# Performance work log

Measured on AMD Instinct MI355X. Metric: run time of the kernel, lower is better.

Reference implementation:

```python
import jax, jax.numpy as jnp
import numpy as np

LN_EPS = 1e-3  # keras LayerNormalization default epsilon


def setup_inputs() -> dict:
    key = jax.random.key(0)
    ks = jax.random.split(key, 6)
    B, S, D, H, K = 4, 4096, 1024, 16, 64
    scale = 1.0 / np.sqrt(D)
    return {
        "x": jax.random.normal(ks[0], (B, S, D), jnp.float32),
        "Wq": jax.random.normal(ks[1], (D, H, K), jnp.float32) * scale,
        "bq": jnp.zeros((H, K), jnp.float32),
        "Wk": jax.random.normal(ks[2], (D, H, K), jnp.float32) * scale,
        "bk": jnp.zeros((H, K), jnp.float32),
        "Wv": jax.random.normal(ks[3], (D, H, K), jnp.float32) * scale,
        "bv": jnp.zeros((H, K), jnp.float32),
        "Wo": jax.random.normal(ks[4], (H, K, D), jnp.float32) * scale,
        "bo": jnp.zeros((D,), jnp.float32),
        "gamma": jnp.ones((D,), jnp.float32),
        "beta": jnp.zeros((D,), jnp.float32),
        "num_window": 8,
    }


def reference(x, Wq, bq, Wk, bk, Wv, bv, Wo, bo, gamma, beta, num_window):
    B, S, D = x.shape
    H, K = Wq.shape[1], Wq.shape[2]
    Sw = S // num_window
    # Block-diagonal (windowed) attention: reshape seq into windows instead of a Python loop.
    xw = x.reshape(B, num_window, Sw, D)  # [B, W, Sw, D]
    q = jnp.einsum('bwsd,dhk->bwshk', xw, Wq) + bq
    k = jnp.einsum('bwsd,dhk->bwshk', xw, Wk) + bk
    v = jnp.einsum('bwsd,dhk->bwshk', xw, Wv) + bv
    scores = jnp.einsum('bwqhk,bwshk->bwhqs', q, k) / jnp.sqrt(jnp.asarray(K, x.dtype))
    attn = jax.nn.softmax(scores, axis=-1)  # [B, W, H, Sw, Sw]
    ctx = jnp.einsum('bwhqs,bwshk->bwqhk', attn, v)
    attn_out = (jnp.einsum('bwqhk,hkd->bwqd', ctx, Wo) + bo).reshape(B, S, D)
    # residual + layernorm (keras eps=1e-3)
    y = x + attn_out
    mu = jnp.mean(y, axis=-1, keepdims=True)
    var = jnp.mean(jnp.square(y - mu), axis=-1, keepdims=True)
    return (y - mu) * jax.lax.rsqrt(var + LN_EPS) * gamma + beta
```

## Files before the change

kernel.cpp:

```cpp
#include <hip/hip_runtime.h>

typedef __bf16 bf16_t;
typedef __bf16 bf16x4 __attribute__((ext_vector_type(4)));
typedef __bf16 bf16x8 __attribute__((ext_vector_type(8)));
typedef float f32x4 __attribute__((ext_vector_type(4)));

#define MFMA16(a, b, c) __builtin_amdgcn_mfma_f32_16x16x32_bf16((a), (b), (c), 0, 0, 0)

#define FENCE asm volatile("" ::: "memory")
#define BAR()                        \
  do {                               \
    FENCE;                           \
    __builtin_amdgcn_s_barrier();    \
    FENCE;                           \
  } while (0)
#define WAITLGKM(n) asm volatile("s_waitcnt lgkmcnt(" #n ")" ::: "memory")

__device__ __forceinline__ void gl_lds16(const bf16_t* g, bf16_t* l) {
  __builtin_amdgcn_global_load_lds(
      (const __attribute__((address_space(1))) void*)g,
      (__attribute__((address_space(3))) void*)l, 16, 0, 0);
}

__global__ __launch_bounds__(256) void cast_x_kernel(const float* __restrict__ x,
                                                     bf16_t* __restrict__ xb) {
  size_t i = (size_t)blockIdx.x * 256 + threadIdx.x;
  float4 v = ((const float4*)x)[i];
  bf16x4 o = {(bf16_t)v.x, (bf16_t)v.y, (bf16_t)v.z, (bf16_t)v.w};
  ((bf16x4*)xb)[i] = o;
}

__global__ __launch_bounds__(256) void transpose_w_kernel(
    const float* __restrict__ Wq, const float* __restrict__ Wk,
    const float* __restrict__ Wv, const float* __restrict__ Wo,
    bf16_t* __restrict__ Wt, bf16_t* __restrict__ WoT) {
  __shared__ bf16_t T[64 * 68];
  const int z = blockIdx.z;
  const float* src = (z == 0) ? Wq : (z == 1) ? Wk : (z == 2) ? Wv : Wo;
  bf16_t* dst = (z < 3) ? (Wt + (size_t)z * 1024 * 1024) : WoT;
  const int tr = blockIdx.y * 64;
  const int tc = blockIdx.x * 64;
  const int tid = threadIdx.x;
#pragma unroll
  for (int it = 0; it < 4; ++it) {
    int t = tid + it * 256;
    int row = t >> 4, c4 = t & 15;
    float4 v = *(const float4*)&src[(size_t)(tr + row) * 1024 + tc + c4 * 4];
    bf16x4 o = {(bf16_t)v.x, (bf16_t)v.y, (bf16_t)v.z, (bf16_t)v.w};
    *(bf16x4*)&T[row * 68 + c4 * 4] = o;
  }
  __syncthreads();
#pragma unroll
  for (int it = 0; it < 2; ++it) {
    int t = tid + it * 256;
    int n = t >> 3, d8 = t & 7;
    bf16x8 o;
#pragma unroll
    for (int j = 0; j < 8; ++j) o[j] = T[(d8 * 8 + j) * 68 + n];
    *(bf16x8*)&dst[(size_t)(tc + n) * 1024 + tr + d8 * 8] = o;
  }
}


__device__ __forceinline__ void stage_half(const bf16_t* __restrict__ g,
                                           bf16_t* l, const int tid) {
#pragma unroll
  for (int j = 0; j < 2; ++j) {
    int idx = j * 512 + tid;
    int row = idx >> 3;
    int c = (idx & 7) ^ (row & 7);
    gl_lds16(g + (size_t)row * 1024 + c * 8, l + idx * 8);
  }
}

__device__ __forceinline__ void tile_step(const int t, bf16_t* const buf,
                                          bf16_t* const nbuf,
                                          const bf16_t* __restrict__ Ab,
                                          const bf16_t* __restrict__ Bb,
                                          f32x4 (&acc)[8][4], const int tid) {
  const int l15 = tid & 15, quad = (tid >> 4) & 3;
  const int wv = tid >> 6, wm = wv >> 2, wn = wv & 3;
  const int sx = l15 & 7;
  const int brow0 = (wn & 1) * 64;
  const bf16_t* const Ar = buf + wm * 8192;
  const bf16_t* const Br = buf + (2 + (wn >> 1)) * 8192;

  bf16x8 af[4][2], bfr[4][2];

#pragma unroll
  for (int nf = 0; nf < 2; ++nf)
#pragma unroll
    for (int ks = 0; ks < 2; ++ks)
      bfr[nf][ks] = *(const bf16x8*)&Br[(brow0 + nf * 16 + l15) * 64 +
                                        (((ks * 4 + quad) ^ sx) << 3)];
  FENCE;
#pragma unroll
  for (int mf = 0; mf < 2; ++mf)
#pragma unroll
    for (int ks = 0; ks < 2; ++ks)
      af[mf][ks] = *(const bf16x8*)&Ar[(mf * 16 + l15) * 64 +
                                       (((ks * 4 + quad) ^ sx) << 3)];
  FENCE;
#pragma unroll
  for (int mf = 2; mf < 4; ++mf)
#pragma unroll
    for (int ks = 0; ks < 2; ++ks)
      af[mf][ks] = *(const bf16x8*)&Ar[(mf * 16 + l15) * 64 +
                                       (((ks * 4 + quad) ^ sx) << 3)];
  FENCE;
#pragma unroll
  for (int nf = 2; nf < 4; ++nf)
#pragma unroll
    for (int ks = 0; ks < 2; ++ks)
      bfr[nf][ks] = *(const bf16x8*)&Br[(brow0 + nf * 16 + l15) * 64 +
                                        (((ks * 4 + quad) ^ sx) << 3)];
  FENCE;
  if (t + 1 < 16) {
    stage_half(Bb + 128 * 1024 + (t + 1) * 64, nbuf + 3 * 8192, tid);
    stage_half(Ab + 128 * 1024 + (t + 1) * 64, nbuf + 1 * 8192, tid);
  }

  WAITLGKM(8);
  __builtin_amdgcn_s_setprio(1);
#pragma unroll
  for (int ks = 0; ks < 2; ++ks)
#pragma unroll
    for (int mf = 0; mf < 2; ++mf)
#pragma unroll
      for (int nf = 0; nf < 2; ++nf)
        acc[mf][nf] = MFMA16(af[mf][ks], bfr[nf][ks], acc[mf][nf]);
  __builtin_amdgcn_s_setprio(0);

  WAITLGKM(4);
  __builtin_amdgcn_s_setprio(1);
#pragma unroll
  for (int ks = 0; ks < 2; ++ks)
#pragma unroll
    for (int mf = 2; mf < 4; ++mf)
#pragma unroll
      for (int nf = 0; nf < 2; ++nf)
        acc[mf][nf] = MFMA16(af[mf][ks], bfr[nf][ks], acc[mf][nf]);
  __builtin_amdgcn_s_setprio(0);

  WAITLGKM(0);
  __builtin_amdgcn_s_setprio(1);
#pragma unroll
  for (int ks = 0; ks < 2; ++ks)
#pragma unroll
    for (int mf = 0; mf < 4; ++mf)
#pragma unroll
      for (int nf = 2; nf < 4; ++nf)
        acc[mf][nf] = MFMA16(af[mf][ks], bfr[nf][ks], acc[mf][nf]);
  __builtin_amdgcn_s_setprio(0);
  BAR();

  if (t + 2 < 16) stage_half(Bb + (t + 2) * 64, buf + 2 * 8192, tid);
#pragma unroll
  for (int mf = 0; mf < 2; ++mf)
#pragma unroll
    for (int ks = 0; ks < 2; ++ks)
      af[mf][ks] = *(const bf16x8*)&Ar[((mf + 4) * 16 + l15) * 64 +
                                       (((ks * 4 + quad) ^ sx) << 3)];
  FENCE;
#pragma unroll
  for (int mf = 2; mf < 4; ++mf)
#pragma unroll
    for (int ks = 0; ks < 2; ++ks)
      af[mf][ks] = *(const bf16x8*)&Ar[((mf + 4) * 16 + l15) * 64 +
                                       (((ks * 4 + quad) ^ sx) << 3)];
  FENCE;
  WAITLGKM(4);
  __builtin_amdgcn_s_setprio(1);
#pragma unroll
  for (int ks = 0; ks < 2; ++ks)
#pragma unroll
    for (int mf = 0; mf < 2; ++mf)
#pragma unroll
      for (int nf = 2; nf < 4; ++nf)
        acc[mf + 4][nf] = MFMA16(af[mf][ks], bfr[nf][ks], acc[mf + 4][nf]);
  __builtin_amdgcn_s_setprio(0);
  WAITLGKM(0);
  __builtin_amdgcn_s_setprio(1);
#pragma unroll
  for (int ks = 0; ks < 2; ++ks)
#pragma unroll
    for (int mf = 2; mf < 4; ++mf)
#pragma unroll
      for (int nf = 2; nf < 4; ++nf)
        acc[mf + 4][nf] = MFMA16(af[mf][ks], bfr[nf][ks], acc[mf + 4][nf]);
  __builtin_amdgcn_s_setprio(0);
  BAR();

  if (t + 2 < 16) stage_half(Ab + (t + 2) * 64, buf + 0 * 8192, tid);
  __builtin_amdgcn_s_setprio(1);
#pragma unroll
  for (int ks = 0; ks < 2; ++ks)
#pragma unroll
    for (int mf = 0; mf < 4; ++mf)
#pragma unroll
      for (int nf = 0; nf < 2; ++nf)
        acc[mf + 4][nf] = MFMA16(af[mf][ks], bfr[nf][ks], acc[mf + 4][nf]);
  __builtin_amdgcn_s_setprio(0);
  if (t < 14)
    asm volatile("s_waitcnt vmcnt(4)" ::: "memory");
  else
    asm volatile("s_waitcnt vmcnt(0)" ::: "memory");
  BAR();
}

__device__ __forceinline__ void gemm256_main(const bf16_t* __restrict__ Ab,
                                             const bf16_t* __restrict__ Bb,
                                             bf16_t* lds, f32x4 (&acc)[8][4],
                                             const int tid) {
  stage_half(Bb, lds + 2 * 8192, tid);
  stage_half(Ab, lds + 0 * 8192, tid);
  stage_half(Bb + 128 * 1024, lds + 3 * 8192, tid);
  stage_half(Ab + 128 * 1024, lds + 1 * 8192, tid);
  stage_half(Bb + 64, lds + 6 * 8192, tid);
  stage_half(Ab + 64, lds + 4 * 8192, tid);
  asm volatile("s_waitcnt vmcnt(4)" ::: "memory");
  BAR();

  for (int t = 0; t < 16; t += 2) {
    tile_step(t, lds, lds + 32768, Ab, Bb, acc, tid);
    tile_step(t + 1, lds + 32768, lds, Ab, Bb, acc, tid);
  }
}

__global__ __launch_bounds__(512, 2) void gemm_qkv_kernel(
    const bf16_t* __restrict__ A, const bf16_t* __restrict__ Bt,
    const float* __restrict__ bq, const float* __restrict__ bk,
    const float* __restrict__ bv, bf16_t* __restrict__ C) {
  __shared__ bf16_t lds[2 * 4 * 8192];
  const int tid = threadIdx.x;
  const int lin = blockIdx.x;
  const int swz = (lin & 7) * 96 + (lin >> 3);
  const int bm = swz / 12, bn = swz - bm * 12;

  f32x4 acc[8][4];
#pragma unroll
  for (int i = 0; i < 8; ++i)
#pragma unroll
    for (int j = 0; j < 4; ++j)
#pragma unroll
      for (int e = 0; e < 4; ++e) acc[i][j][e] = 0.f;

  gemm256_main(A + (size_t)(bm * 256) * 1024, Bt + (size_t)(bn * 256) * 1024,
               lds, acc, tid);

  const int l15 = tid & 15, quad = (tid >> 4) & 3;
  const int wv = tid >> 6, wm = wv >> 2, wn = wv & 3;
  const int col0 = bn * 256 + wn * 64;
  const int rbase = bm * 256 + wm * 128;
  float* R = (float*)(lds + wv * 8192);

  float wbias[4], wscale[4];
#pragma unroll
  for (int nf = 0; nf < 4; ++nf) {
    int col = col0 + nf * 16 + l15;
    if (col < 1024) {
      wbias[nf] = bq[col];
      wscale[nf] = 0.125f;
    } else if (col < 2048) {
      wbias[nf] = bk[col - 1024];
      wscale[nf] = 1.f;
    } else {
      wbias[nf] = bv[col - 2048];
      wscale[nf] = 1.f;
    }
  }
#pragma unroll
  for (int p = 0; p < 4; ++p) {
#pragma unroll
    for (int mfi = 0; mfi < 2; ++mfi) {
#pragma unroll
      for (int nf = 0; nf < 4; ++nf)
#pragma unroll
        for (int r = 0; r < 4; ++r)
          R[(mfi * 16 + quad * 4 + r) * 68 + nf * 16 + l15] =
              (acc[p * 2 + mfi][nf][r] + wbias[nf]) * wscale[nf];
    }
    WAITLGKM(0);
#pragma unroll
    for (int i = 0; i < 8; ++i) {
      const int lr = i * 4 + quad;
      f32x4 vv = *(const f32x4*)&R[lr * 68 + l15 * 4];
      bf16x4 o = {(bf16_t)vv[0], (bf16_t)vv[1], (bf16_t)vv[2], (bf16_t)vv[3]};
      int row = rbase + p * 32 + lr;
      *(bf16x4*)&C[(size_t)row * 3072 + col0 + l15 * 4] = o;
    }
    WAITLGKM(0);
  }
}

__global__ __launch_bounds__(256) void attn_kernel(
    const bf16_t* __restrict__ QKV, bf16_t* __restrict__ Ctx) {
  __shared__ bf16_t Ks[2][64 * 64];
  __shared__ bf16_t Vs[2][64 * 64];
  __shared__ bf16_t Pb[4][16 * 64];

  const int tid = threadIdx.x;
  const int wv = tid >> 6, quad = (tid >> 4) & 3, l15 = tid & 15;
  const int hid = blockIdx.x, qb = blockIdx.y;
  const int b = hid >> 7, w = (hid >> 4) & 7, h = hid & 15;
  const int rowW = b * 4096 + w * 512;
  const int qbase = qb * 128 + wv * 32;

  bf16x8 qf[2][2];
#pragma unroll
  for (int qt = 0; qt < 2; ++qt) {
    int rowQ = rowW + qbase + qt * 16 + l15;
#pragma unroll
    for (int kh = 0; kh < 2; ++kh)
      qf[qt][kh] = *(const bf16x8*)&QKV[(size_t)rowQ * 3072 + h * 64 + kh * 32 + quad * 8];
  }

  const bf16_t* Kb = QKV + (size_t)rowW * 3072 + 1024 + h * 64;
  const bf16_t* Vg = QKV + (size_t)rowW * 3072 + 2048 + h * 64;

  float lp[2] = {0.f, 0.f};
  f32x4 Oa[2][4];
  f32x4 zero = {0.f, 0.f, 0.f, 0.f};
#pragma unroll
  for (int qt = 0; qt < 2; ++qt)
#pragma unroll
    for (int dt = 0; dt < 4; ++dt) Oa[qt][dt] = zero;

  const int vrow = tid >> 2;
  const int vseg = tid & 3;
  const int sg = vrow >> 3, sr = vrow & 7;

  bf16x8 vr0, vr1;
  {
    const bf16_t* src = Vg + (size_t)vrow * 3072 + vseg * 16;
    vr0 = *(const bf16x8*)&src[0];
    vr1 = *(const bf16x8*)&src[8];
  }
  FENCE;
#pragma unroll
  for (int i = 0; i < 2; ++i) {
    int t = tid + i * 256;
    int row = t >> 3;
    int g = (t & 7) ^ (row & 7);
    gl_lds16(Kb + (size_t)row * 3072 + g * 8, &Ks[0][t * 8]);
  }
  FENCE;

#pragma unroll 2
  for (int kt = 0; kt < 8; ++kt) {
    const int cb = kt & 1;
    bf16x8 vn0 = vr0, vn1 = vr1;
    if (kt < 7) {
      const bf16_t* src = Vg + (size_t)((kt + 1) * 64 + vrow) * 3072 + vseg * 16;
      vn0 = *(const bf16x8*)&src[0];
      vn1 = *(const bf16x8*)&src[8];
      FENCE;
#pragma unroll
      for (int i = 0; i < 2; ++i) {
        int t = tid + i * 256;
        int row = t >> 3;
        int g = (t & 7) ^ (row & 7);
        gl_lds16(Kb + (size_t)((kt + 1) * 64 + row) * 3072 + g * 8, &Ks[cb ^ 1][t * 8]);
      }
      asm volatile("s_waitcnt vmcnt(4)" ::: "memory");
    } else {
      asm volatile("s_waitcnt vmcnt(0)" ::: "memory");
    }
#pragma unroll
    for (int j = 0; j < 8; ++j) {
      int d0 = vseg * 16 + j;
      Vs[cb][d0 * 64 + ((sg ^ (d0 & 7)) << 3) + sr] = vr0[j];
      int d1 = vseg * 16 + 8 + j;
      Vs[cb][d1 * 64 + ((sg ^ (d1 & 7)) << 3) + sr] = vr1[j];
    }
    WAITLGKM(0);
    BAR();

    bf16x8 kf[4][2], vf[2][4];
#pragma unroll
    for (int jt = 0; jt < 4; ++jt) {
      int key = jt * 16 + l15;
#pragma unroll
      for (int kh = 0; kh < 2; ++kh)
        kf[jt][kh] = *(const bf16x8*)&Ks[cb][key * 64 + (((kh * 4 + quad) ^ (key & 7)) << 3)];
    }
#pragma unroll
    for (int kh = 0; kh < 2; ++kh)
#pragma unroll
      for (int dt = 0; dt < 4; ++dt) {
        int d = dt * 16 + l15;
        vf[kh][dt] = *(const bf16x8*)&Vs[cb][d * 64 + (((kh * 4 + quad) ^ (d & 7)) << 3)];
      }

#pragma unroll
    for (int qt = 0; qt < 2; ++qt) {
      f32x4 st[4];
#pragma unroll
      for (int jt = 0; jt < 4; ++jt) {
        f32x4 a = zero;
#pragma unroll
        for (int kh = 0; kh < 2; ++kh) a = MFMA16(kf[jt][kh], qf[qt][kh], a);
        st[jt] = a;
      }
      float ls = 0.f;
#pragma unroll
      for (int jt = 0; jt < 4; ++jt)
#pragma unroll
        for (int r = 0; r < 4; ++r) {
          float p = __expf(st[jt][r]);
          st[jt][r] = p;
          ls += p;
        }
      lp[qt] += ls;
#pragma unroll
      for (int jt = 0; jt < 4; ++jt) {
        bf16x4 pk = {(bf16_t)st[jt][0], (bf16_t)st[jt][1],
                     (bf16_t)st[jt][2], (bf16_t)st[jt][3]};
        int gs = (jt * 2 + (quad >> 1)) ^ (l15 & 7);
        *(bf16x4*)&Pb[wv][l15 * 64 + gs * 8 + (quad & 1) * 4] = pk;
      }
#pragma unroll
      for (int kh = 0; kh < 2; ++kh) {
        bf16x8 pf = *(const bf16x8*)&Pb[wv][l15 * 64 + (((kh * 4 + quad) ^ (l15 & 7)) << 3)];
#pragma unroll
        for (int dt = 0; dt < 4; ++dt) Oa[qt][dt] = MFMA16(pf, vf[kh][dt], Oa[qt][dt]);
      }
    }
    WAITLGKM(0);
    BAR();
    vr0 = vn0;
    vr1 = vn1;
  }

#pragma unroll
  for (int qt = 0; qt < 2; ++qt) {
    float t = lp[qt];
    t += __shfl_xor(t, 16, 64);
    t += __shfl_xor(t, 32, 64);
    float inv_l = 1.0f / t;
    float inv[4];
#pragma unroll
    for (int r = 0; r < 4; ++r) inv[r] = __shfl(inv_l, quad * 4 + r, 64);
#pragma unroll
    for (int dt = 0; dt < 4; ++dt)
#pragma unroll
      for (int r = 0; r < 4; ++r) {
        int orow = rowW + qbase + qt * 16 + quad * 4 + r;
        Ctx[(size_t)orow * 1024 + h * 64 + dt * 16 + l15] = (bf16_t)(Oa[qt][dt][r] * inv[r]);
      }
  }
}

__global__ __launch_bounds__(512, 2) void gemm_proj_kernel(
    const bf16_t* __restrict__ A, const bf16_t* __restrict__ Bt,
    const float* __restrict__ bo, const float* __restrict__ x,
    bf16_t* __restrict__ Yb) {
  __shared__ bf16_t lds[2 * 4 * 8192];
  const int tid = threadIdx.x;
  const int lin = blockIdx.x;
  const int swz = (lin & 7) * 32 + (lin >> 3);
  const int bm = swz >> 2, bn = swz & 3;

  f32x4 acc[8][4];
#pragma unroll
  for (int i = 0; i < 8; ++i)
#pragma unroll
    for (int j = 0; j < 4; ++j)
#pragma unroll
      for (int e = 0; e < 4; ++e) acc[i][j][e] = 0.f;

  gemm256_main(A + (size_t)(bm * 256) * 1024, Bt + (size_t)(bn * 256) * 1024,
               lds, acc, tid);

  const int l15 = tid & 15, quad = (tid >> 4) & 3;
  const int wv = tid >> 6, wm = wv >> 2, wn = wv & 3;
  const int col0 = bn * 256 + wn * 64;
  const int rbase = bm * 256 + wm * 128;
  float* R = (float*)(lds + wv * 8192);
  const int colg = col0 + l15 * 4;
  const float4 bo4 = *(const float4*)&bo[colg];

#pragma unroll
  for (int p = 0; p < 4; ++p) {
#pragma unroll
    for (int mfi = 0; mfi < 2; ++mfi) {
#pragma unroll
      for (int nf = 0; nf < 4; ++nf)
#pragma unroll
        for (int r = 0; r < 4; ++r)
          R[(mfi * 16 + quad * 4 + r) * 68 + nf * 16 + l15] = acc[p * 2 + mfi][nf][r];
    }
    WAITLGKM(0);
#pragma unroll
    for (int i = 0; i < 8; ++i) {
      const int lr = i * 4 + quad;
      int row = rbase + p * 32 + lr;
      f32x4 vv = *(const f32x4*)&R[lr * 68 + l15 * 4];
      float4 xv = *(const float4*)&x[(size_t)row * 1024 + colg];
      bf16x4 o = {(bf16_t)(vv[0] + bo4.x + xv.x), (bf16_t)(vv[1] + bo4.y + xv.y),
                  (bf16_t)(vv[2] + bo4.z + xv.z), (bf16_t)(vv[3] + bo4.w + xv.w)};
      *(bf16x4*)&Yb[(size_t)row * 1024 + colg] = o;
    }
    WAITLGKM(0);
  }
}

__global__ __launch_bounds__(256) void ln_kernel(const bf16_t* __restrict__ Yb,
                                                 float* __restrict__ Y,
                                                 const float* __restrict__ gamma,
                                                 const float* __restrict__ beta) {
  const int row = blockIdx.x, tid = threadIdx.x;
  bf16x4 yb = ((const bf16x4*)(Yb + (size_t)row * 1024))[tid];
  float y0 = (float)yb[0], y1 = (float)yb[1], y2 = (float)yb[2], y3 = (float)yb[3];
  float s = y0 + y1 + y2 + y3;
  float s2 = y0 * y0 + y1 * y1 + y2 * y2 + y3 * y3;
#pragma unroll
  for (int off = 1; off < 64; off <<= 1) {
    s += __shfl_xor(s, off, 64);
    s2 += __shfl_xor(s2, off, 64);
  }
  __shared__ float red[8];
  int wv = tid >> 6;
  if ((tid & 63) == 0) {
    red[wv] = s;
    red[4 + wv] = s2;
  }
  __syncthreads();
  s = red[0] + red[1] + red[2] + red[3];
  s2 = red[4] + red[5] + red[6] + red[7];
  float mean = s * (1.0f / 1024.0f);
  float var = s2 * (1.0f / 1024.0f) - mean * mean;
  float rs = rsqrtf(var + 1e-3f);
  float4 g = ((const float4*)gamma)[tid];
  float4 bb = ((const float4*)beta)[tid];
  float4 o;
  o.x = (y0 - mean) * rs * g.x + bb.x;
  o.y = (y1 - mean) * rs * g.y + bb.y;
  o.z = (y2 - mean) * rs * g.z + bb.z;
  o.w = (y3 - mean) * rs * g.w + bb.w;
  ((float4*)(Y + (size_t)row * 1024))[tid] = o;
}

extern "C" void kernel_launch(void* const* d_in, const int* in_sizes, int n_in,
                              void* d_out, int out_size, void* d_ws, size_t ws_size,
                              hipStream_t stream) {
  const float* x = (const float*)d_in[0];
  const float* Wq = (const float*)d_in[1];
  const float* bq = (const float*)d_in[2];
  const float* Wk = (const float*)d_in[3];
  const float* bk = (const float*)d_in[4];
  const float* Wv = (const float*)d_in[5];
  const float* bv = (const float*)d_in[6];
  const float* Wo = (const float*)d_in[7];
  const float* bo = (const float*)d_in[8];
  const float* gamma = (const float*)d_in[9];
  const float* beta = (const float*)d_in[10];
  float* Y = (float*)d_out;

  char* ws = (char*)d_ws;
  bf16_t* xb = (bf16_t*)(ws);
  bf16_t* Wt = (bf16_t*)(ws + 33554432);
  bf16_t* WoT = (bf16_t*)(ws + 39845888);
  bf16_t* QKVb = (bf16_t*)(ws + 41943040);
  bf16_t* Ctx = (bf16_t*)(ws + 142606336);
  bf16_t* Yb = (bf16_t*)(ws + 176160768);

  cast_x_kernel<<<16384, 256, 0, stream>>>(x, xb);
  transpose_w_kernel<<<dim3(16, 16, 4), 256, 0, stream>>>(Wq, Wk, Wv, Wo, Wt, WoT);
  gemm_qkv_kernel<<<768, 512, 0, stream>>>(xb, Wt, bq, bk, bv, QKVb);
  attn_kernel<<<dim3(512, 4), 256, 0, stream>>>(QKVb, Ctx);
  gemm_proj_kernel<<<256, 512, 0, stream>>>(Ctx, WoT, bo, x, Yb);
  ln_kernel<<<16384, 256, 0, stream>>>(Yb, Y, gamma, beta);
}
```

Measured before the change: 365.9 us.

## Restructure GEMM main-loop interleaving with extra barriers and swizzle attention grid

```diff
diff --git a/kernel.cpp b/kernel.cpp
--- a/kernel.cpp
+++ b/kernel.cpp
@@ -95,19 +95,27 @@
                                         (((ks * 4 + quad) ^ sx) << 3)];
   FENCE;
 #pragma unroll
-  for (int mf = 0; mf < 2; ++mf)
+  for (int mf = 0; mf < 4; ++mf)
 #pragma unroll
     for (int ks = 0; ks < 2; ++ks)
       af[mf][ks] = *(const bf16x8*)&Ar[(mf * 16 + l15) * 64 +
                                        (((ks * 4 + quad) ^ sx) << 3)];
   FENCE;
-#pragma unroll
-  for (int mf = 2; mf < 4; ++mf)
-#pragma unroll
-    for (int ks = 0; ks < 2; ++ks)
-      af[mf][ks] = *(const bf16x8*)&Ar[(mf * 16 + l15) * 64 +
-                                       (((ks * 4 + quad) ^ sx) << 3)];
-  FENCE;
+  if (t + 1 < 16) stage_half(Bb + 128 * 1024 + (t + 1) * 64, nbuf + 3 * 8192, tid);
+  WAITLGKM(8);
+  BAR();
+  WAITLGKM(0);
+  __builtin_amdgcn_s_setprio(1);
+#pragma unroll
+  for (int ks = 0; ks < 2; ++ks)
+#pragma unroll
+    for (int mf = 0; mf < 4; ++mf)
+#pragma unroll
+      for (int nf = 0; nf < 2; ++nf)
+        acc[mf][nf] = MFMA16(af[mf][ks], bfr[nf][ks], acc[mf][nf]);
+  __builtin_amdgcn_s_setprio(0);
+  BAR();
+
 #pragma unroll
   for (int nf = 2; nf < 4; ++nf)
 #pragma unroll
@@ -115,33 +123,8 @@
       bfr[nf][ks] = *(const bf16x8*)&Br[(brow0 + nf * 16 + l15) * 64 +
                                         (((ks * 4 + quad) ^ sx) << 3)];
   FENCE;
-  if (t + 1 < 16) {
-    stage_half(Bb + 128 * 1024 + (t + 1) * 64, nbuf + 3 * 8192, tid);
-    stage_half(Ab + 128 * 1024 + (t + 1) * 64, nbuf + 1 * 8192, tid);
-  }
-
-  WAITLGKM(8);
-  __builtin_amdgcn_s_setprio(1);
-#pragma unroll
-  for (int ks = 0; ks < 2; ++ks)
-#pragma unroll
-    for (int mf = 0; mf < 2; ++mf)
-#pragma unroll
-      for (int nf = 0; nf < 2; ++nf)
-        acc[mf][nf] = MFMA16(af[mf][ks], bfr[nf][ks], acc[mf][nf]);
-  __builtin_amdgcn_s_setprio(0);
-
-  WAITLGKM(4);
-  __builtin_amdgcn_s_setprio(1);
-#pragma unroll
-  for (int ks = 0; ks < 2; ++ks)
-#pragma unroll
-    for (int mf = 2; mf < 4; ++mf)
-#pragma unroll
-      for (int nf = 0; nf < 2; ++nf)
-        acc[mf][nf] = MFMA16(af[mf][ks], bfr[nf][ks], acc[mf][nf]);
-  __builtin_amdgcn_s_setprio(0);
-
+  if (t + 1 < 16) stage_half(Ab + 128 * 1024 + (t + 1) * 64, nbuf + 1 * 8192, tid);
+  BAR();
   WAITLGKM(0);
   __builtin_amdgcn_s_setprio(1);
 #pragma unroll
@@ -154,44 +137,29 @@
   __builtin_amdgcn_s_setprio(0);
   BAR();
 
-  if (t + 2 < 16) stage_half(Bb + (t + 2) * 64, buf + 2 * 8192, tid);
-#pragma unroll
-  for (int mf = 0; mf < 2; ++mf)
+#pragma unroll
+  for (int mf = 0; mf < 4; ++mf)
 #pragma unroll
     for (int ks = 0; ks < 2; ++ks)
       af[mf][ks] = *(const bf16x8*)&Ar[((mf + 4) * 16 + l15) * 64 +
                                        (((ks * 4 + quad) ^ sx) << 3)];
   FENCE;
-#pragma unroll
-  for (int mf = 2; mf < 4; ++mf)
-#pragma unroll
-    for (int ks = 0; ks < 2; ++ks)
-      af[mf][ks] = *(const bf16x8*)&Ar[((mf + 4) * 16 + l15) * 64 +
-                                       (((ks * 4 + quad) ^ sx) << 3)];
-  FENCE;
-  WAITLGKM(4);
+  if (t + 2 < 16) stage_half(Bb + (t + 2) * 64, buf + 2 * 8192, tid);
+  BAR();
+  WAITLGKM(0);
   __builtin_amdgcn_s_setprio(1);
 #pragma unroll
   for (int ks = 0; ks < 2; ++ks)
 #pragma unroll
-    for (int mf = 0; mf < 2; ++mf)
+    for (int mf = 0; mf < 4; ++mf)
 #pragma unroll
       for (int nf = 2; nf < 4; ++nf)
         acc[mf + 4][nf] = MFMA16(af[mf][ks], bfr[nf][ks], acc[mf + 4][nf]);
   __builtin_amdgcn_s_setprio(0);
-  WAITLGKM(0);
-  __builtin_amdgcn_s_setprio(1);
-#pragma unroll
-  for (int ks = 0; ks < 2; ++ks)
-#pragma unroll
-    for (int mf = 2; mf < 4; ++mf)
-#pragma unroll
-      for (int nf = 2; nf < 4; ++nf)
-        acc[mf + 4][nf] = MFMA16(af[mf][ks], bfr[nf][ks], acc[mf + 4][nf]);
-  __builtin_amdgcn_s_setprio(0);
   BAR();
 
   if (t + 2 < 16) stage_half(Ab + (t + 2) * 64, buf + 0 * 8192, tid);
+  BAR();
   __builtin_amdgcn_s_setprio(1);
 #pragma unroll
   for (int ks = 0; ks < 2; ++ks)
@@ -301,7 +269,9 @@
 
   const int tid = threadIdx.x;
   const int wv = tid >> 6, quad = (tid >> 4) & 3, l15 = tid & 15;
-  const int hid = blockIdx.x, qb = blockIdx.y;
+  const int lin = blockIdx.x;
+  const int swz = (lin & 7) * 256 + (lin >> 3);
+  const int hid = swz >> 2, qb = swz & 3;
   const int b = hid >> 7, w = (hid >> 4) & 7, h = hid & 15;
   const int rowW = b * 4096 + w * 512;
   const int qbase = qb * 128 + wv * 32;
@@ -568,7 +538,7 @@
   cast_x_kernel<<<16384, 256, 0, stream>>>(x, xb);
   transpose_w_kernel<<<dim3(16, 16, 4), 256, 0, stream>>>(Wq, Wk, Wv, Wo, Wt, WoT);
   gemm_qkv_kernel<<<768, 512, 0, stream>>>(xb, Wt, bq, bk, bv, QKVb);
-  attn_kernel<<<dim3(512, 4), 256, 0, stream>>>(QKVb, Ctx);
+  attn_kernel<<<2048, 256, 0, stream>>>(QKVb, Ctx);
   gemm_proj_kernel<<<256, 512, 0, stream>>>(Ctx, WoT, bo, x, Yb);
   ln_kernel<<<16384, 256, 0, stream>>>(Yb, Y, gamma, beta);
 }
```

Measured after the change: 376.4 us. +2.9%, slower.
